# Optimization experiments

Measured on AMD Instinct MI355X. Metric: run time of the kernel, lower is better.

Reference implementation:

```python
import jax, jax.numpy as jnp
import numpy as np

TARGETS_COUNT = 8
TARGET_LEN = 256
BATCH = 32


def setup_inputs() -> dict:
    key = jax.random.key(0)
    target = jax.random.normal(key, (BATCH, TARGETS_COUNT, TARGET_LEN), dtype=jnp.float32)
    return {"target": target}


def _bispectrum(x):
    # x: [L].  TM[l1, l2] = (1/L) * sum_n x[n] * x[n-l1] * x[n-l2],
    # where x[k] = 0 for k < 0 (zero left-padding, non-circular).
    L = x.shape[0]
    n = jnp.arange(L)
    idx = n[None, :] - n[:, None]            # idx[l, n] = n - l
    S = jnp.where(idx >= 0, x[jnp.clip(idx, 0, L - 1)], jnp.float32(0))  # S[l, n] = x[n-l]
    # TM[l1, l2] = sum_n (x[n] * S[l1, n]) * S[l2, n]
    return ((S * x[None, :]) @ S.T) / L      # [L, L]


def reference(target):
    # target: [B, T, L] -> bispectrum per signal, averaged over T.
    bs = jax.vmap(jax.vmap(_bispectrum))(target)      # [B, T, L, L]
    source = jnp.mean(bs, axis=1)[:, None, :, :]       # [B, 1, L, L]
    return source, target
```

## Files before the change

kernel.cpp:

```cpp
#include <hip/hip_runtime.h>


typedef short bf16x8 __attribute__((ext_vector_type(8)));
typedef float f32x4 __attribute__((ext_vector_type(4)));

#define LEN 256
#define NT 8

static __device__ __forceinline__ bf16x8 mk8(uint a0, uint a1, uint a2, uint a3) {
    union { uint u[4]; bf16x8 v; } c;
    c.u[0] = a0; c.u[1] = a1; c.u[2] = a2; c.u[3] = a3;
    return c.v;
}

static __device__ __forceinline__ uint packsplit(float v) {
    uint u  = __float_as_uint(v);
    uint hb = (u + 0x7fffu + ((u >> 16) & 1u)) >> 16;
    float hf = __uint_as_float(hb << 16);
    float lf = v - hf;
    uint lb = __float_as_uint(lf);
    uint lo = (lb + 0x7fffu + ((lb >> 16) & 1u)) >> 16;
    return hb | (lo << 16);
}

static __device__ __forceinline__ float unpackf(uint p) {
    return __uint_as_float(p << 16) + __uint_as_float(p & 0xffff0000u);
}

__global__ __launch_bounds__(256, 2) void bispec_mfma(const float* __restrict__ x,
                                                      float* __restrict__ out) {
    __shared__ uint smem[8704];

    const int b   = blockIdx.z;
    const int tid = threadIdx.x;
    const int w   = tid >> 6;
    const int l   = tid & 63;
    const int cg  = l & 15;
    const int g   = l >> 4;
    const int l1b = blockIdx.x << 6;
    const int l2b = blockIdx.y << 6;

    const float* xb = x + b * (NT * LEN);
    for (int i = tid; i < 4096; i += 256) {
        int j = i & 511;
        float v = (j >= 256) ? xb[(i >> 9) * 256 + (j - 256)] : 0.0f;
        uint p = packsplit(v);
        smem[i]        = p;
        smem[4097 + i] = p;
    }
    __syncthreads();

    f32x4 acc[4][4];
    #pragma unroll
    for (int mi = 0; mi < 4; ++mi)
        #pragma unroll
        for (int ni = 0; ni < 4; ++ni)
            acc[mi][ni] = 0.0f;

    for (int tt = 0; tt < 2; ++tt) {
        const int t   = w + tt * 4;
        const int tB  = t * 512 + 256;
        const int qA0 = tB + g * 8 - l1b - cg;
        const int qB0 = tB + g * 8 - l2b - cg;
        const int xnb = tB + g * 8;

        for (int kb = 0; kb < 8; ++kb) {
            const uint4 xp0 = *(const uint4*)&smem[xnb + kb * 32];
            const uint4 xp1 = *(const uint4*)&smem[xnb + kb * 32 + 4];
            const float xn[8] = {unpackf(xp0.x), unpackf(xp0.y), unpackf(xp0.z), unpackf(xp0.w),
                                 unpackf(xp1.x), unpackf(xp1.y), unpackf(xp1.z), unpackf(xp1.w)};

            uint Ah[4][4], Al[4][4], Bh[4][4], Bl[4][4];

            #pragma unroll
            for (int mi = 0; mi < 4; ++mi) {
                int q0 = qA0 + kb * 32 - mi * 16;
                int ad = q0 + (q0 & 1) * 4097;
                const uint2 d0 = *(const uint2*)&smem[ad];
                const uint2 d1 = *(const uint2*)&smem[ad + 2];
                const uint2 d2 = *(const uint2*)&smem[ad + 4];
                const uint2 d3 = *(const uint2*)&smem[ad + 6];
                const uint sd[8] = {d0.x, d0.y, d1.x, d1.y, d2.x, d2.y, d3.x, d3.y};
                #pragma unroll
                for (int p = 0; p < 4; ++p) {
                    float a0 = xn[2*p]     * unpackf(sd[2*p]);
                    float a1 = xn[2*p + 1] * unpackf(sd[2*p + 1]);
                    uint u0 = __float_as_uint(a0);
                    uint h0 = (u0 + 0x7fffu + ((u0 >> 16) & 1u)) >> 16;
                    uint u1 = __float_as_uint(a1);
                    uint h1 = (u1 + 0x7fffu + ((u1 >> 16) & 1u)) >> 16;
                    Ah[mi][p] = h0 | (h1 << 16);
                    float e0 = a0 - __uint_as_float(h0 << 16);
                    float e1 = a1 - __uint_as_float(h1 << 16);
                    Al[mi][p] = (__float_as_uint(e0) >> 16) | (__float_as_uint(e1) & 0xffff0000u);
                }
            }

            #pragma unroll
            for (int ni = 0; ni < 4; ++ni) {
                int p0 = qB0 + kb * 32 - ni * 16;
                int ad = p0 + (p0 & 1) * 4097;
                const uint2 d0 = *(const uint2*)&smem[ad];
                const uint2 d1 = *(const uint2*)&smem[ad + 2];
                const uint2 d2 = *(const uint2*)&smem[ad + 4];
                const uint2 d3 = *(const uint2*)&smem[ad + 6];
                Bh[ni][0] = (d0.x & 0xffffu) | (d0.y << 16);
                Bl[ni][0] = (d0.x >> 16)     | (d0.y & 0xffff0000u);
                Bh[ni][1] = (d1.x & 0xffffu) | (d1.y << 16);
                Bl[ni][1] = (d1.x >> 16)     | (d1.y & 0xffff0000u);
                Bh[ni][2] = (d2.x & 0xffffu) | (d2.y << 16);
                Bl[ni][2] = (d2.x >> 16)     | (d2.y & 0xffff0000u);
                Bh[ni][3] = (d3.x & 0xffffu) | (d3.y << 16);
                Bl[ni][3] = (d3.x >> 16)     | (d3.y & 0xffff0000u);
            }

            #pragma unroll
            for (int mi = 0; mi < 4; ++mi) {
                const bf16x8 ah = mk8(Ah[mi][0], Ah[mi][1], Ah[mi][2], Ah[mi][3]);
                const bf16x8 al = mk8(Al[mi][0], Al[mi][1], Al[mi][2], Al[mi][3]);
                #pragma unroll
                for (int ni = 0; ni < 4; ++ni) {
                    const bf16x8 bh = mk8(Bh[ni][0], Bh[ni][1], Bh[ni][2], Bh[ni][3]);
                    const bf16x8 bl = mk8(Bl[ni][0], Bl[ni][1], Bl[ni][2], Bl[ni][3]);
                    acc[mi][ni] = __builtin_amdgcn_mfma_f32_16x16x32_bf16(ah, bh, acc[mi][ni], 0, 0, 0);
                    acc[mi][ni] = __builtin_amdgcn_mfma_f32_16x16x32_bf16(ah, bl, acc[mi][ni], 0, 0, 0);
                    acc[mi][ni] = __builtin_amdgcn_mfma_f32_16x16x32_bf16(al, bh, acc[mi][ni], 0, 0, 0);
                }
            }
        }
    }

    __syncthreads();
    float* red0 = (float*)smem;
    float* red1 = (float*)(smem + 4352);

    if (w == 2) {
        #pragma unroll
        for (int mi = 0; mi < 4; ++mi)
            #pragma unroll
            for (int ni = 0; ni < 4; ++ni)
                #pragma unroll
                for (int q = 0; q < 4; ++q)
                    red0[(mi*16 + g*4 + q)*68 + ni*16 + cg] = acc[mi][ni][q];
    }
    if (w == 3) {
        #pragma unroll
        for (int mi = 0; mi < 4; ++mi)
            #pragma unroll
            for (int ni = 0; ni < 4; ++ni)
                #pragma unroll
                for (int q = 0; q < 4; ++q)
                    red1[(mi*16 + g*4 + q)*68 + ni*16 + cg] = acc[mi][ni][q];
    }
    __syncthreads();
    if (w == 0) {
        #pragma unroll
        for (int mi = 0; mi < 4; ++mi)
            #pragma unroll
            for (int ni = 0; ni < 4; ++ni)
                #pragma unroll
                for (int q = 0; q < 4; ++q)
                    acc[mi][ni][q] += red0[(mi*16 + g*4 + q)*68 + ni*16 + cg];
    }
    if (w == 1) {
        #pragma unroll
        for (int mi = 0; mi < 4; ++mi)
            #pragma unroll
            for (int ni = 0; ni < 4; ++ni)
                #pragma unroll
                for (int q = 0; q < 4; ++q)
                    acc[mi][ni][q] += red1[(mi*16 + g*4 + q)*68 + ni*16 + cg];
    }
    __syncthreads();
    if (w == 1) {
        #pragma unroll
        for (int mi = 0; mi < 4; ++mi)
            #pragma unroll
            for (int ni = 0; ni < 4; ++ni)
                #pragma unroll
                for (int q = 0; q < 4; ++q)
                    red0[(mi*16 + g*4 + q)*68 + ni*16 + cg] = acc[mi][ni][q];
    }
    __syncthreads();
    if (w == 0) {
        const float s = 1.0f / (float)(LEN * NT);
        float* ob = out + (size_t)b * LEN * LEN;
        #pragma unroll
        for (int mi = 0; mi < 4; ++mi)
            #pragma unroll
            for (int ni = 0; ni < 4; ++ni)
                #pragma unroll
                for (int q = 0; q < 4; ++q) {
                    float v = acc[mi][ni][q] + red0[(mi*16 + g*4 + q)*68 + ni*16 + cg];
                    ob[(size_t)(l1b + mi*16 + g*4 + q) * LEN + (l2b + ni*16 + cg)] = v * s;
                }
    }
}

extern "C" void kernel_launch(void* const* d_in, const int* in_sizes, int n_in,
                              void* d_out, int out_size, void* d_ws, size_t ws_size,
                              hipStream_t stream) {
    const float* x = (const float*)d_in[0];
    float* out = (float*)d_out;

    dim3 grid(4, 4, 32);
    bispec_mfma<<<grid, dim3(256), 0, stream>>>(x, out);

    hipMemcpyAsync(out + (size_t)32 * LEN * LEN, x,
                   (size_t)32 * NT * LEN * sizeof(float),
                   hipMemcpyDeviceToDevice, stream);
}
```

Baseline: 91.09 us.

## Exploit bispectrum symmetry and zero padding with split-K blocks plus reduce kernel

After: 88.99 us. -2.3%, faster.

```diff
diff --git a/kernel.cpp b/kernel.cpp
--- a/kernel.cpp
+++ b/kernel.cpp
@@ -1,52 +1,76 @@
 #include <hip/hip_runtime.h>
 
-
-typedef short bf16x8 __attribute__((ext_vector_type(8)));
-typedef float f32x4 __attribute__((ext_vector_type(4)));
 
 #define LEN 256
 #define NT 8
-
-static __device__ __forceinline__ bf16x8 mk8(uint a0, uint a1, uint a2, uint a3) {
-    union { uint u[4]; bf16x8 v; } c;
-    c.u[0] = a0; c.u[1] = a1; c.u[2] = a2; c.u[3] = a3;
-    return c.v;
-}
-
-static __device__ __forceinline__ uint packsplit(float v) {
-    uint u  = __float_as_uint(v);
-    uint hb = (u + 0x7fffu + ((u >> 16) & 1u)) >> 16;
-    float hf = __uint_as_float(hb << 16);
-    float lf = v - hf;
-    uint lb = __float_as_uint(lf);
-    uint lo = (lb + 0x7fffu + ((lb >> 16) & 1u)) >> 16;
-    return hb | (lo << 16);
-}
-
-static __device__ __forceinline__ float unpackf(uint p) {
-    return __uint_as_float(p << 16) + __uint_as_float(p & 0xffff0000u);
-}
-
-__global__ __launch_bounds__(256, 2) void bispec_mfma(const float* __restrict__ x,
-                                                      float* __restrict__ out) {
-    __shared__ uint smem[8704];
-
-    const int b   = blockIdx.z;
+#define F1OFF 4113
+#define REDSTR 68
+#define SMEM_DW 8704
+
+typedef _Float16 f16x8 __attribute__((ext_vector_type(8)));
+typedef float    f32x4 __attribute__((ext_vector_type(4)));
+
+__constant__ uchar4 kBlockTab[20] = {
+    {0,0,0,0},{0,0,2,0},{0,0,4,0},{0,0,6,0},
+    {1,0,2,0},{1,0,4,0},{1,0,6,0},
+    {1,1,2,0},{1,1,4,0},{1,1,6,0},
+    {2,0,4,0},{2,0,6,0},
+    {2,1,4,0},{2,1,6,0},
+    {2,2,4,0},{2,2,6,0},
+    {3,0,6,0},{3,1,6,0},{3,2,6,0},{3,3,6,0}};
+__constant__ uchar4 kPairTab[10] = {
+    {0,0,0,4},{1,0,4,3},{1,1,7,3},{2,0,10,2},{2,1,12,2},{2,2,14,2},
+    {3,0,16,1},{3,1,17,1},{3,2,18,1},{3,3,19,1}};
+
+static __device__ __forceinline__ void split2(float a0, float a1, uint& hb, uint& lb) {
+    auto h = __builtin_amdgcn_cvt_pkrtz(a0, a1);
+    float e0 = a0 - (float)h[0];
+    float e1 = a1 - (float)h[1];
+    auto e = __builtin_amdgcn_cvt_pkrtz(e0, e1);
+    __builtin_memcpy(&hb, &h, 4);
+    __builtin_memcpy(&lb, &e, 4);
+}
+static __device__ __forceinline__ f16x8 mkf(const uint* u) {
+    f16x8 v;
+    __builtin_memcpy(&v, u, 16);
+    return v;
+}
+static __device__ __forceinline__ void readwin(const float* fs, int p0, float* wv) {
+    const float* bp = fs + p0 + ((p0 & 1) ? F1OFF : 0);
+    float2 d0 = *(const float2*)bp;
+    float2 d1 = *(const float2*)(bp + 2);
+    float2 d2 = *(const float2*)(bp + 4);
+    float2 d3 = *(const float2*)(bp + 6);
+    wv[0] = d0.x; wv[1] = d0.y; wv[2] = d1.x; wv[3] = d1.y;
+    wv[4] = d2.x; wv[5] = d2.y; wv[6] = d3.x; wv[7] = d3.y;
+}
+
+__global__ __launch_bounds__(256, 3) void bispec_main(const float* __restrict__ x,
+                                                      float* __restrict__ dst,
+                                                      int partial) {
+    __shared__ float fs[SMEM_DW];
+    const int b  = blockIdx.y;
+    const int bx = blockIdx.x;
+
+    int ti, tj, kb0, kbn;
+    if (partial) {
+        uchar4 e = kBlockTab[bx];
+        ti = e.x; tj = e.y; kb0 = e.z; kbn = 2;
+    } else {
+        ti = bx >> 2; tj = bx & 3;
+        int m = ti > tj ? ti : tj;
+        kb0 = 2 * m; kbn = 8 - 2 * m;
+    }
+    const int l1b = ti << 6, l2b = tj << 6;
     const int tid = threadIdx.x;
-    const int w   = tid >> 6;
-    const int l   = tid & 63;
-    const int cg  = l & 15;
-    const int g   = l >> 4;
-    const int l1b = blockIdx.x << 6;
-    const int l2b = blockIdx.y << 6;
+    const int w = tid >> 6, l = tid & 63, cg = l & 15, g = l >> 4;
 
     const float* xb = x + b * (NT * LEN);
     for (int i = tid; i < 4096; i += 256) {
         int j = i & 511;
         float v = (j >= 256) ? xb[(i >> 9) * 256 + (j - 256)] : 0.0f;
-        uint p = packsplit(v);
-        smem[i]        = p;
-        smem[4097 + i] = p;
+        fs[i] = v;
+        fs[F1OFF + i] = v;
     }
     __syncthreads();
 
@@ -54,103 +78,79 @@
     #pragma unroll
     for (int mi = 0; mi < 4; ++mi)
         #pragma unroll
-        for (int ni = 0; ni < 4; ++ni)
-            acc[mi][ni] = 0.0f;
+        for (int ni = 0; ni < 4; ++ni) acc[mi][ni] = 0.0f;
 
     for (int tt = 0; tt < 2; ++tt) {
-        const int t   = w + tt * 4;
-        const int tB  = t * 512 + 256;
-        const int qA0 = tB + g * 8 - l1b - cg;
-        const int qB0 = tB + g * 8 - l2b - cg;
-        const int xnb = tB + g * 8;
-
-        for (int kb = 0; kb < 8; ++kb) {
-            const uint4 xp0 = *(const uint4*)&smem[xnb + kb * 32];
-            const uint4 xp1 = *(const uint4*)&smem[xnb + kb * 32 + 4];
-            const float xn[8] = {unpackf(xp0.x), unpackf(xp0.y), unpackf(xp0.z), unpackf(xp0.w),
-                                 unpackf(xp1.x), unpackf(xp1.y), unpackf(xp1.z), unpackf(xp1.w)};
-
-            uint Ah[4][4], Al[4][4], Bh[4][4], Bl[4][4];
-
+        const int t  = w + tt * 4;
+        const int tB = t * 512 + 256;
+        const int cA = tB + g * 8 - l1b - cg;
+        const int cB = tB + g * 8 - l2b - cg;
+        const int cX = tB + g * 8;
+
+        for (int kb = kb0; kb < kb0 + kbn; ++kb) {
+            const float4 x0 = *(const float4*)&fs[cX + kb * 32];
+            const float4 x1 = *(const float4*)&fs[cX + kb * 32 + 4];
+            const float xn[8] = {x0.x, x0.y, x0.z, x0.w, x1.x, x1.y, x1.z, x1.w};
+
+            f16x8 ah[4], al[4];
             #pragma unroll
             for (int mi = 0; mi < 4; ++mi) {
-                int q0 = qA0 + kb * 32 - mi * 16;
-                int ad = q0 + (q0 & 1) * 4097;
-                const uint2 d0 = *(const uint2*)&smem[ad];
-                const uint2 d1 = *(const uint2*)&smem[ad + 2];
-                const uint2 d2 = *(const uint2*)&smem[ad + 4];
-                const uint2 d3 = *(const uint2*)&smem[ad + 6];
-                const uint sd[8] = {d0.x, d0.y, d1.x, d1.y, d2.x, d2.y, d3.x, d3.y};
-                #pragma unroll
-                for (int p = 0; p < 4; ++p) {
-                    float a0 = xn[2*p]     * unpackf(sd[2*p]);
-                    float a1 = xn[2*p + 1] * unpackf(sd[2*p + 1]);
-                    uint u0 = __float_as_uint(a0);
-                    uint h0 = (u0 + 0x7fffu + ((u0 >> 16) & 1u)) >> 16;
-                    uint u1 = __float_as_uint(a1);
-                    uint h1 = (u1 + 0x7fffu + ((u1 >> 16) & 1u)) >> 16;
-                    Ah[mi][p] = h0 | (h1 << 16);
-                    float e0 = a0 - __uint_as_float(h0 << 16);
-                    float e1 = a1 - __uint_as_float(h1 << 16);
-                    Al[mi][p] = (__float_as_uint(e0) >> 16) | (__float_as_uint(e1) & 0xffff0000u);
-                }
+                float wv[8];
+                readwin(fs, cA + kb * 32 - mi * 16, wv);
+                uint Ahp[4], Alp[4];
+                #pragma unroll
+                for (int p = 0; p < 4; ++p)
+                    split2(xn[2 * p] * wv[2 * p], xn[2 * p + 1] * wv[2 * p + 1],
+                           Ahp[p], Alp[p]);
+                ah[mi] = mkf(Ahp); al[mi] = mkf(Alp);
             }
 
             #pragma unroll
             for (int ni = 0; ni < 4; ++ni) {
-                int p0 = qB0 + kb * 32 - ni * 16;
-                int ad = p0 + (p0 & 1) * 4097;
-                const uint2 d0 = *(const uint2*)&smem[ad];
-                const uint2 d1 = *(const uint2*)&smem[ad + 2];
-                const uint2 d2 = *(const uint2*)&smem[ad + 4];
-                const uint2 d3 = *(const uint2*)&smem[ad + 6];
-                Bh[ni][0] = (d0.x & 0xffffu) | (d0.y << 16);
-                Bl[ni][0] = (d0.x >> 16)     | (d0.y & 0xffff0000u);
-                Bh[ni][1] = (d1.x & 0xffffu) | (d1.y << 16);
-                Bl[ni][1] = (d1.x >> 16)     | (d1.y & 0xffff0000u);
-                Bh[ni][2] = (d2.x & 0xffffu) | (d2.y << 16);
-                Bl[ni][2] = (d2.x >> 16)     | (d2.y & 0xffff0000u);
-                Bh[ni][3] = (d3.x & 0xffffu) | (d3.y << 16);
-                Bl[ni][3] = (d3.x >> 16)     | (d3.y & 0xffff0000u);
-            }
-
-            #pragma unroll
-            for (int mi = 0; mi < 4; ++mi) {
-                const bf16x8 ah = mk8(Ah[mi][0], Ah[mi][1], Ah[mi][2], Ah[mi][3]);
-                const bf16x8 al = mk8(Al[mi][0], Al[mi][1], Al[mi][2], Al[mi][3]);
-                #pragma unroll
-                for (int ni = 0; ni < 4; ++ni) {
-                    const bf16x8 bh = mk8(Bh[ni][0], Bh[ni][1], Bh[ni][2], Bh[ni][3]);
-                    const bf16x8 bl = mk8(Bl[ni][0], Bl[ni][1], Bl[ni][2], Bl[ni][3]);
-                    acc[mi][ni] = __builtin_amdgcn_mfma_f32_16x16x32_bf16(ah, bh, acc[mi][ni], 0, 0, 0);
-                    acc[mi][ni] = __builtin_amdgcn_mfma_f32_16x16x32_bf16(ah, bl, acc[mi][ni], 0, 0, 0);
-                    acc[mi][ni] = __builtin_amdgcn_mfma_f32_16x16x32_bf16(al, bh, acc[mi][ni], 0, 0, 0);
+                float wv[8];
+                readwin(fs, cB + kb * 32 - ni * 16, wv);
+                uint Bhp[4], Blp[4];
+                #pragma unroll
+                for (int p = 0; p < 4; ++p)
+                    split2(wv[2 * p], wv[2 * p + 1], Bhp[p], Blp[p]);
+                const f16x8 bh = mkf(Bhp), bl = mkf(Blp);
+                #pragma unroll
+                for (int mi = 0; mi < 4; ++mi) {
+                    acc[mi][ni] = __builtin_amdgcn_mfma_f32_16x16x32_f16(ah[mi], bh, acc[mi][ni], 0, 0, 0);
+                    acc[mi][ni] = __builtin_amdgcn_mfma_f32_16x16x32_f16(ah[mi], bl, acc[mi][ni], 0, 0, 0);
+                    acc[mi][ni] = __builtin_amdgcn_mfma_f32_16x16x32_f16(al[mi], bh, acc[mi][ni], 0, 0, 0);
                 }
             }
         }
     }
 
     __syncthreads();
-    float* red0 = (float*)smem;
-    float* red1 = (float*)(smem + 4352);
-
-    if (w == 2) {
-        #pragma unroll
-        for (int mi = 0; mi < 4; ++mi)
-            #pragma unroll
-            for (int ni = 0; ni < 4; ++ni)
-                #pragma unroll
-                for (int q = 0; q < 4; ++q)
-                    red0[(mi*16 + g*4 + q)*68 + ni*16 + cg] = acc[mi][ni][q];
-    }
-    if (w == 3) {
-        #pragma unroll
-        for (int mi = 0; mi < 4; ++mi)
-            #pragma unroll
-            for (int ni = 0; ni < 4; ++ni)
-                #pragma unroll
-                for (int q = 0; q < 4; ++q)
-                    red1[(mi*16 + g*4 + q)*68 + ni*16 + cg] = acc[mi][ni][q];
+    float* buf0 = fs;
+    float* buf1 = fs + 4352;
+    if (w >= 2) {
+        float* bb = (w == 2) ? buf0 : buf1;
+        #pragma unroll
+        for (int mi = 0; mi < 4; ++mi)
+            #pragma unroll
+            for (int ni = 0; ni < 4; ++ni)
+                *(f32x4*)&bb[(ni * 16 + cg) * REDSTR + mi * 16 + g * 4] = acc[mi][ni];
+    }
+    __syncthreads();
+    if (w < 2) {
+        float* bb = (w == 0) ? buf0 : buf1;
+        #pragma unroll
+        for (int mi = 0; mi < 4; ++mi)
+            #pragma unroll
+            for (int ni = 0; ni < 4; ++ni)
+                acc[mi][ni] += *(f32x4*)&bb[(ni * 16 + cg) * REDSTR + mi * 16 + g * 4];
+    }
+    __syncthreads();
+    if (w == 1) {
+        #pragma unroll
+        for (int mi = 0; mi < 4; ++mi)
+            #pragma unroll
+            for (int ni = 0; ni < 4; ++ni)
+                *(f32x4*)&buf0[(ni * 16 + cg) * REDSTR + mi * 16 + g * 4] = acc[mi][ni];
     }
     __syncthreads();
     if (w == 0) {
@@ -158,42 +158,47 @@
         for (int mi = 0; mi < 4; ++mi)
             #pragma unroll
             for (int ni = 0; ni < 4; ++ni)
-                #pragma unroll
-                for (int q = 0; q < 4; ++q)
-                    acc[mi][ni][q] += red0[(mi*16 + g*4 + q)*68 + ni*16 + cg];
-    }
-    if (w == 1) {
-        #pragma unroll
-        for (int mi = 0; mi < 4; ++mi)
-            #pragma unroll
-            for (int ni = 0; ni < 4; ++ni)
-                #pragma unroll
-                for (int q = 0; q < 4; ++q)
-                    acc[mi][ni][q] += red1[(mi*16 + g*4 + q)*68 + ni*16 + cg];
-    }
-    __syncthreads();
-    if (w == 1) {
-        #pragma unroll
-        for (int mi = 0; mi < 4; ++mi)
-            #pragma unroll
-            for (int ni = 0; ni < 4; ++ni)
-                #pragma unroll
-                for (int q = 0; q < 4; ++q)
-                    red0[(mi*16 + g*4 + q)*68 + ni*16 + cg] = acc[mi][ni][q];
-    }
-    __syncthreads();
-    if (w == 0) {
-        const float s = 1.0f / (float)(LEN * NT);
-        float* ob = out + (size_t)b * LEN * LEN;
-        #pragma unroll
-        for (int mi = 0; mi < 4; ++mi)
-            #pragma unroll
-            for (int ni = 0; ni < 4; ++ni)
-                #pragma unroll
-                for (int q = 0; q < 4; ++q) {
-                    float v = acc[mi][ni][q] + red0[(mi*16 + g*4 + q)*68 + ni*16 + cg];
-                    ob[(size_t)(l1b + mi*16 + g*4 + q) * LEN + (l2b + ni*16 + cg)] = v * s;
-                }
+                acc[mi][ni] += *(f32x4*)&buf0[(ni * 16 + cg) * REDSTR + mi * 16 + g * 4];
+
+        if (partial) {
+            float* ob = dst + ((size_t)b * 20 + bx) * 4096;
+            #pragma unroll
+            for (int mi = 0; mi < 4; ++mi)
+                #pragma unroll
+                for (int ni = 0; ni < 4; ++ni)
+                    #pragma unroll
+                    for (int q = 0; q < 4; ++q)
+                        ob[(mi * 16 + g * 4 + q) * 64 + ni * 16 + cg] = acc[mi][ni][q];
+        } else {
+            float* ob = dst + (size_t)b * (LEN * LEN);
+            const float s = 1.0f / (float)(LEN * NT);
+            #pragma unroll
+            for (int mi = 0; mi < 4; ++mi)
+                #pragma unroll
+                for (int ni = 0; ni < 4; ++ni)
+                    #pragma unroll
+                    for (int q = 0; q < 4; ++q)
+                        ob[(size_t)(l1b + mi * 16 + g * 4 + q) * LEN + l2b + ni * 16 + cg] =
+                            acc[mi][ni][q] * s;
+        }
+    }
+}
+
+__global__ __launch_bounds__(256) void bispec_reduce(const float* __restrict__ ws,
+                                                     float* __restrict__ out) {
+    const int p = blockIdx.x, b = blockIdx.y;
+    uchar4 e = kPairTab[p];
+    const int ii = e.x, jj = e.y, s = e.z, c = e.w;
+    const float* base = ws + ((size_t)b * 20 + s) * 4096;
+    float* ob = out + (size_t)b * (LEN * LEN);
+    const float scale = 1.0f / (float)(LEN * NT);
+    for (int k = threadIdx.x; k < 4096; k += 256) {
+        float v = base[k];
+        for (int q = 1; q < c; ++q) v += base[(size_t)q * 4096 + k];
+        v *= scale;
+        int r = k >> 6, cc = k & 63;
+        ob[(ii * 64 + r) * LEN + jj * 64 + cc] = v;
+        if (ii != jj) ob[(jj * 64 + cc) * LEN + ii * 64 + r] = v;
     }
 }
 
@@ -203,10 +208,16 @@
     const float* x = (const float*)d_in[0];
     float* out = (float*)d_out;
 
-    dim3 grid(4, 4, 32);
-    bispec_mfma<<<grid, dim3(256), 0, stream>>>(x, out);
-
-    hipMemcpyAsync(out + (size_t)32 * LEN * LEN, x,
-                   (size_t)32 * NT * LEN * sizeof(float),
-                   hipMemcpyDeviceToDevice, stream);
-}
+    const size_t ws_need = (size_t)32 * 20 * 4096 * sizeof(float);
+    if (ws_size >= ws_need) {
+        float* ws = (float*)d_ws;
+        bispec_main<<<dim3(20, 32), dim3(256), 0, stream>>>(x, ws, 1);
+        bispec_reduce<<<dim3(10, 32), dim3(256), 0, stream>>>(ws, out);
+    } else {
+        bispec_main<<<dim3(16, 32), dim3(256), 0, stream>>>(x, out, 0);
+    }
+
+    (void)hipMemcpyAsync(out + (size_t)32 * LEN * LEN, x,
+                         (size_t)32 * NT * LEN * sizeof(float),
+                         hipMemcpyDeviceToDevice, stream);
+}
```
